# Performance work log

Measured on AMD Instinct MI355X. Metric: run time of the kernel, lower is better.

The kernel has to match this reference:

```python
import jax, jax.numpy as jnp
import numpy as np
from jax import lax

KSIZE, STRIDE, RATE, FUSE_K, SCALE, FUSE = 3, 1, 2, 3, 10.0, True


def _same_pad(h, w, k, s):
    oh, ow = -(-h // s), -(-w // s)
    ph = max(0, (oh - 1) * s + k - h)
    pw = max(0, (ow - 1) * s + k - w)
    return (ph // 2, ph - ph // 2), (pw // 2, pw - pw // 2), oh, ow


def extract_patches(x, k, s):
    # x: [B,C,H,W] -> ([B, L, C, k, k], Ho, Wo); matches torch Unfold with 'same' padding
    B, C, H, W = x.shape
    (pt, pb), (pl, pr), Ho, Wo = _same_pad(H, W, k, s)
    xp = jnp.pad(x, ((0, 0), (0, 0), (pt, pb), (pl, pr)))
    rows = []
    for i in range(k):
        cols = [xp[:, :, i:i + s * (Ho - 1) + 1:s, j:j + s * (Wo - 1) + 1:s] for j in range(k)]
        rows.append(jnp.stack(cols, axis=2))  # [B,C,k,Ho,Wo]
    pat = jnp.stack(rows, axis=2)  # [B,C,k,k,Ho,Wo]
    pat = pat.reshape(B, C, k, k, Ho * Wo).transpose(0, 4, 1, 2, 3)
    return pat, Ho, Wo


def setup_inputs() -> dict:
    key = jax.random.key(0)
    kf, kb = jax.random.split(key)
    f = jax.random.normal(kf, (2, 128, 64, 64), dtype=jnp.float32)
    b = jax.random.normal(kb, (2, 128, 64, 64), dtype=jnp.float32)
    mask = jnp.zeros((2, 1, 256, 256), dtype=jnp.float32)
    return {"f": f, "b": b, "mask": mask}


def _forward(f, b, mask):
    B, C, Hr, Wr = f.shape
    kernel = 2 * RATE
    # raw background patches used as deconv kernels: [B, L, C, 4, 4]
    raw_w, _, _ = extract_patches(b, kernel, RATE * STRIDE)
    # nearest 1/rate downsample (torch nearest picks every rate-th pixel)
    fd = f[:, :, ::RATE, ::RATE]
    bd = b[:, :, ::RATE, ::RATE]
    Hf, Wf = fd.shape[2], fd.shape[3]
    Hb, Wb = bd.shape[2], bd.shape[3]
    L = Hb * Wb
    w, _, _ = extract_patches(bd, KSIZE, STRIDE)  # [B, L, C, 3, 3]
    # mask -> validity per background patch (original uses batch 0's mask only)
    md = mask[:, :, ::4 * RATE, ::4 * RATE]
    m, _, _ = extract_patches(md, KSIZE, STRIDE)  # [B, L, 1, 3, 3]
    mm = (jnp.mean(m[0], axis=(1, 2, 3)) == 0.0).astype(f.dtype)  # [L]
    # l2-normalize patch kernels (escape_NaN added per element before sum, as in torch)
    wn = w / jnp.sqrt(jnp.sum(w * w + 1e-4, axis=(2, 3, 4), keepdims=True))
    # correlation conv == batched GEMM over extracted foreground patches
    fp, _, _ = extract_patches(fd, KSIZE, 1)  # [B, P=Hf*Wf, C, 3, 3]
    scores = jnp.einsum('bpckl,bqckl->bqp', fp, wn)  # [B, L, Hf*Wf]
    scores = scores.reshape(B, Hb, Wb, Hf, Wf)

    if FUSE:
        def fuse_diag(y2):  # conv with 3x3 identity kernel, same pad == 3 diagonal shifts
            yp = jnp.pad(y2, ((1, 1), (1, 1)))
            return yp[:-2, :-2] + yp[1:-1, 1:-1] + yp[2:, 2:]

        def fuse_one(s):  # [Hb,Wb,Hf,Wf]
            y = fuse_diag(s.reshape(Hb * Wb, Hf * Wf)).reshape(Hb, Wb, Hf, Wf)
            y = y.transpose(1, 0, 3, 2)
            y = fuse_diag(y.reshape(Wb * Hb, Wf * Hf)).reshape(Wb, Hb, Wf, Hf)
            return y.transpose(1, 0, 3, 2)

        scores = jax.vmap(fuse_one)(scores)

    yi = scores.reshape(B, L, Hf, Wf) * mm[None, :, None, None]
    yi = jax.nn.softmax(yi * SCALE, axis=1) * mm[None, :, None, None]

    # transposed conv with per-batch raw patches as kernels (stride=rate, padding=1), /4
    def deconv_one(attn, wpat):  # attn [L,Hf,Wf], wpat [L,C,4,4]
        rhs = jnp.flip(wpat, axis=(2, 3)).transpose(1, 0, 2, 3)  # [C, L, 4, 4]
        pad = kernel - 1 - 1  # equivalent VALID padding for transposed conv with padding=1
        out = lax.conv_general_dilated(attn[None], rhs, (1, 1),
                                       padding=((pad, pad), (pad, pad)),
                                       lhs_dilation=(RATE, RATE),
                                       dimension_numbers=('NCHW', 'OIHW', 'NCHW'))
        return out[0] / 4.0

    y = jax.vmap(deconv_one)(yi, raw_w)  # [B, C, Hr, Wr]
    return y


def reference(f, b, mask):
    return _forward(f, b, mask)
```

## Files before the change

kernel.cpp:

```cpp
#include <hip/hip_runtime.h>
#include <hip/hip_bf16.h>
#include <math.h>

constexpr int HS = 32;
constexpr int Lq = 1024;
constexpr int CN = 128;

typedef short bf16x8 __attribute__((ext_vector_type(8)));
typedef float f32x4  __attribute__((ext_vector_type(4)));

__device__ inline unsigned short f2bf(float x) {
    union { float f; unsigned int u; } c; c.f = x;
    return (unsigned short)((c.u + 0x7FFF + ((c.u >> 16) & 1)) >> 16);
}
__device__ inline float bf2f(unsigned short h) {
    union { unsigned int u; float f; } c; c.u = ((unsigned int)h) << 16;
    return c.f;
}

__global__ __launch_bounds__(64) void k_prep2(const float* __restrict__ f,
                                              const float* __restrict__ bsrc,
                                              unsigned short* __restrict__ fH, unsigned short* __restrict__ fL,
                                              unsigned short* __restrict__ bH, unsigned short* __restrict__ bL,
                                              float* __restrict__ ssq) {
    int u = blockIdx.x;
    int tx = threadIdx.x;
    int p = u & (Lq - 1), bb = u >> 10;
    int py = p >> 5, px = p & 31;
    long srcbase = (((long)bb * CN) * 64 + 2 * py) * 64 + 2 * px;
    float s = 0.f;
#pragma unroll
    for (int i = 0; i < 2; ++i) {
        int c = tx + i * 64;
        long src = srcbase + (long)c * 4096;
        float fv = f[src], bv = bsrc[src];
        int o = u * CN + c;
        unsigned short fh = f2bf(fv), bh = f2bf(bv);
        fH[o] = fh; fL[o] = f2bf(fv - bf2f(fh));
        bH[o] = bh; bL[o] = f2bf(bv - bf2f(bh));
        s += bv * bv;
    }
    for (int off = 32; off > 0; off >>= 1) s += __shfl_down(s, off, 64);
    if (tx == 0) ssq[u] = s;
}

__global__ __launch_bounds__(256) void k_nm(const float* __restrict__ ssq, const float* __restrict__ mask,
                                            float* __restrict__ norms, float* __restrict__ mmb) {
    int idx = blockIdx.x * 256 + threadIdx.x;
    if (idx < 2048) {
        int q = idx & (Lq - 1);
        int bb = idx >> 10;
        int qy = q >> 5, qx = q & 31;
        float s = 0.1152f;
        for (int dk = -1; dk <= 1; ++dk) {
            int y = qy + dk; if ((unsigned)y >= (unsigned)HS) continue;
            for (int dl = -1; dl <= 1; ++dl) {
                int x = qx + dl; if ((unsigned)x >= (unsigned)HS) continue;
                s += ssq[bb * Lq + y * HS + x];
            }
        }
        norms[idx] = sqrtf(s);
    } else {
        int q = idx - 2048;
        int qy = q >> 5, qx = q & 31;
        float s = 0.f;
        for (int dk = -1; dk <= 1; ++dk) {
            int y = qy + dk; if ((unsigned)y >= (unsigned)HS) continue;
            for (int dl = -1; dl <= 1; ++dl) {
                int x = qx + dl; if ((unsigned)x >= (unsigned)HS) continue;
                s += mask[(8 * y) * 256 + 8 * x];
            }
        }
        mmb[q] = (s == 0.0f) ? 1.0f : 0.0f;
    }
}

__global__ __launch_bounds__(256) void k_gram(const unsigned short* __restrict__ fH,
                                              const unsigned short* __restrict__ fL,
                                              const unsigned short* __restrict__ bH,
                                              const unsigned short* __restrict__ bL,
                                              float* __restrict__ GT) {
    const long bz = blockIdx.z;
    const unsigned short* AH = fH + bz * 131072;
    const unsigned short* AL = fL + bz * 131072;
    const unsigned short* BH = bH + bz * 131072;
    const unsigned short* BL = bL + bz * 131072;
    float* C = GT + (bz << 20);
    int t = threadIdx.x, w = t >> 6, lane = t & 63, quad = lane >> 4, l16 = lane & 15;
    int wm = blockIdx.x * 64 + (w & 1) * 32;
    int wn = blockIdx.y * 64 + (w >> 1) * 32;
    int ko = quad * 8;
    f32x4 acc[2][2] = {};
#pragma unroll
    for (int k0 = 0; k0 < 128; k0 += 32) {
        bf16x8 ah0 = *(const bf16x8*)&AH[(wm + l16) * 128 + ko + k0];
        bf16x8 ah1 = *(const bf16x8*)&AH[(wm + 16 + l16) * 128 + ko + k0];
        bf16x8 al0 = *(const bf16x8*)&AL[(wm + l16) * 128 + ko + k0];
        bf16x8 al1 = *(const bf16x8*)&AL[(wm + 16 + l16) * 128 + ko + k0];
        bf16x8 bh0 = *(const bf16x8*)&BH[(wn + l16) * 128 + ko + k0];
        bf16x8 bh1 = *(const bf16x8*)&BH[(wn + 16 + l16) * 128 + ko + k0];
        bf16x8 bl0 = *(const bf16x8*)&BL[(wn + l16) * 128 + ko + k0];
        bf16x8 bl1 = *(const bf16x8*)&BL[(wn + 16 + l16) * 128 + ko + k0];
        acc[0][0] = __builtin_amdgcn_mfma_f32_16x16x32_bf16(ah0, bh0, acc[0][0], 0, 0, 0);
        acc[0][1] = __builtin_amdgcn_mfma_f32_16x16x32_bf16(ah0, bh1, acc[0][1], 0, 0, 0);
        acc[1][0] = __builtin_amdgcn_mfma_f32_16x16x32_bf16(ah1, bh0, acc[1][0], 0, 0, 0);
        acc[1][1] = __builtin_amdgcn_mfma_f32_16x16x32_bf16(ah1, bh1, acc[1][1], 0, 0, 0);
        acc[0][0] = __builtin_amdgcn_mfma_f32_16x16x32_bf16(ah0, bl0, acc[0][0], 0, 0, 0);
        acc[0][1] = __builtin_amdgcn_mfma_f32_16x16x32_bf16(ah0, bl1, acc[0][1], 0, 0, 0);
        acc[1][0] = __builtin_amdgcn_mfma_f32_16x16x32_bf16(ah1, bl0, acc[1][0], 0, 0, 0);
        acc[1][1] = __builtin_amdgcn_mfma_f32_16x16x32_bf16(ah1, bl1, acc[1][1], 0, 0, 0);
        acc[0][0] = __builtin_amdgcn_mfma_f32_16x16x32_bf16(al0, bh0, acc[0][0], 0, 0, 0);
        acc[0][1] = __builtin_amdgcn_mfma_f32_16x16x32_bf16(al0, bh1, acc[0][1], 0, 0, 0);
        acc[1][0] = __builtin_amdgcn_mfma_f32_16x16x32_bf16(al1, bh0, acc[1][0], 0, 0, 0);
        acc[1][1] = __builtin_amdgcn_mfma_f32_16x16x32_bf16(al1, bh1, acc[1][1], 0, 0, 0);
    }
#pragma unroll
    for (int i = 0; i < 2; ++i)
#pragma unroll
        for (int j = 0; j < 2; ++j) {
            int mrow = wm + i * 16 + quad * 4;
            int ncol = wn + j * 16 + l16;
#pragma unroll
            for (int r = 0; r < 4; ++r)
                C[(long)(mrow + r) * Lq + ncol] = acc[i][j][r];
        }
}

__global__ __launch_bounds__(256) void k_s0T(const float* __restrict__ GT, const float* __restrict__ norms,
                                             float* __restrict__ S0T) {
    int idx = blockIdx.x * 256 + threadIdx.x;
    int q  = idx & (Lq - 1);
    int pp = (idx >> 10) & (Lq - 1);
    int bb = idx >> 20;
    int qy = q >> 5, qx = q & 31, py = pp >> 5, px = pp & 31;
    const float* Gb = GT + ((long)bb << 20);
    float s = 0.f;
#pragma unroll
    for (int dk = -1; dk <= 1; ++dk) {
        if ((unsigned)(qy + dk) >= (unsigned)HS || (unsigned)(py + dk) >= (unsigned)HS) continue;
#pragma unroll
        for (int dl = -1; dl <= 1; ++dl) {
            if ((unsigned)(qx + dl) >= (unsigned)HS || (unsigned)(px + dl) >= (unsigned)HS) continue;
            int sft = dk * HS + dl;
            s += Gb[(long)(pp + sft) * Lq + (q + sft)];
        }
    }
    S0T[idx] = s / norms[bb * Lq + q];
}

__global__ __launch_bounds__(256) void k_fuse12(const float* __restrict__ S0, float* __restrict__ S2) {
    int idx = blockIdx.x * 256 + threadIdx.x;
    int p  = idx & (Lq - 1);
    int q  = (idx >> 10) & (Lq - 1);
    int bb = idx >> 20;
    int hb = q >> 5, wb = q & 31, hf = p >> 5, wf = p & 31;
    int ip = wb * HS + hb, jp = wf * HS + hf;
    const float* S = S0 + (long)bb * Lq * Lq;
    float s = 0.f;
#pragma unroll
    for (int d = -1; d <= 1; ++d) {
        int t = ip + d, r = jp + d;
        if ((unsigned)t < (unsigned)Lq && (unsigned)r < (unsigned)Lq) {
            int q2 = (t & 31) * HS + (t >> 5);
            int p2 = (r & 31) * HS + (r >> 5);
            long base = (long)q2 * Lq + p2;
            float v = S[base];
            if (q2 > 0 && p2 > 0)             v += S[base - (Lq + 1)];
            if (q2 < Lq - 1 && p2 < Lq - 1)   v += S[base + (Lq + 1)];
            s += v;
        }
    }
    S2[idx] = s;
}

__global__ __launch_bounds__(256) void k_softmaxT(const float* __restrict__ S2T, const float* __restrict__ mmb,
                                                  unsigned short* __restrict__ At) {
    int wid = blockIdx.x * 4 + (threadIdx.x >> 6);
    int lane = threadIdx.x & 63;
    int bb = wid >> 10, p = wid & (Lq - 1);
    const float* row = S2T + ((long)bb << 20) + (long)p * Lq;
    unsigned short* orow = At + ((long)bb << 20) + (long)p * Lq;
    float x[16]; float mx = -1e30f;
#pragma unroll
    for (int i = 0; i < 16; ++i) {
        int q = i * 64 + lane;
        x[i] = row[q] * mmb[q] * 10.0f;
        mx = fmaxf(mx, x[i]);
    }
    for (int off = 32; off > 0; off >>= 1) mx = fmaxf(mx, __shfl_xor(mx, off, 64));
    float e[16]; float s = 0.f;
#pragma unroll
    for (int i = 0; i < 16; ++i) { e[i] = __expf(x[i] - mx); s += e[i]; }
    for (int off = 32; off > 0; off >>= 1) s += __shfl_xor(s, off, 64);
    float inv = 1.0f / s;
#pragma unroll
    for (int i = 0; i < 16; ++i) {
        int q = i * 64 + lane;
        orow[q] = f2bf(e[i] * mmb[q] * inv);
    }
}

__global__ __launch_bounds__(256) void k_wm(const float* __restrict__ bsrc, unsigned short* __restrict__ Wm) {
    int idx = blockIdx.x * 256 + threadIdx.x;
    int q  = idx & (Lq - 1);
    int m  = (idx >> 10) & 2047;
    int bb = idx >> 21;
    int c = m >> 4, u = (m >> 2) & 3, v = m & 3;
    int qy = q >> 5, qx = q & 31;
    int y = 2 * qy + u - 1, x = 2 * qx + v - 1;
    float val = 0.f;
    if ((unsigned)y < 64u && (unsigned)x < 64u)
        val = bsrc[(((long)bb * CN + c) * 64 + y) * 64 + x];
    Wm[idx] = f2bf(val);
}

__global__ __launch_bounds__(256) void k_gemm_mfma(const unsigned short* __restrict__ WmA,
                                                   const unsigned short* __restrict__ At,
                                                   float* __restrict__ Cm) {
    const long bz = blockIdx.z;
    const unsigned short* A = WmA + bz * (2048L * Lq);
    const unsigned short* B = At  + bz * ((long)Lq * Lq);
    float* C = Cm + bz * (2048L * Lq);
    __shared__ __align__(16) unsigned short Bs[4096];
    int t = threadIdx.x;
    int w = t >> 6, lane = t & 63;
    int quad = lane >> 4, l16 = lane & 15;
    int m0 = blockIdx.x * 64, n0 = blockIdx.y * 64;
    const unsigned short* aS = A + (long)(m0 + w * 16 + l16) * Lq + quad * 8;
    const unsigned short* bS = B + (long)(n0 + w * 16 + l16) * Lq + quad * 8;
    int sidx = w * 512 + quad * 128 + l16 * 8;
    int fidx = quad * 128 + l16 * 8;
    f32x4 acc0 = {0,0,0,0}, acc1 = {0,0,0,0}, acc2 = {0,0,0,0}, acc3 = {0,0,0,0};
    for (int k0 = 0; k0 < Lq; k0 += 64) {
        bf16x8 bv0 = *(const bf16x8*)(bS + k0);
        bf16x8 bv1 = *(const bf16x8*)(bS + k0 + 32);
        bf16x8 af0 = *(const bf16x8*)(aS + k0);
        bf16x8 af1 = *(const bf16x8*)(aS + k0 + 32);
        __syncthreads();
        *(bf16x8*)&Bs[sidx]        = bv0;
        *(bf16x8*)&Bs[2048 + sidx] = bv1;
        __syncthreads();
#pragma unroll
        for (int kc = 0; kc < 2; ++kc) {
            int o = kc * 2048;
            bf16x8 af = kc ? af1 : af0;
            bf16x8 b0 = *(const bf16x8*)&Bs[o + fidx];
            bf16x8 b1 = *(const bf16x8*)&Bs[o + 512 + fidx];
            bf16x8 b2 = *(const bf16x8*)&Bs[o + 1024 + fidx];
            bf16x8 b3 = *(const bf16x8*)&Bs[o + 1536 + fidx];
            acc0 = __builtin_amdgcn_mfma_f32_16x16x32_bf16(af, b0, acc0, 0, 0, 0);
            acc1 = __builtin_amdgcn_mfma_f32_16x16x32_bf16(af, b1, acc1, 0, 0, 0);
            acc2 = __builtin_amdgcn_mfma_f32_16x16x32_bf16(af, b2, acc2, 0, 0, 0);
            acc3 = __builtin_amdgcn_mfma_f32_16x16x32_bf16(af, b3, acc3, 0, 0, 0);
        }
    }
    int mrow = m0 + w * 16 + quad * 4;
#pragma unroll
    for (int r = 0; r < 4; ++r) {
        C[(long)(mrow + r) * Lq + n0 +  0 + l16] = acc0[r];
        C[(long)(mrow + r) * Lq + n0 + 16 + l16] = acc1[r];
        C[(long)(mrow + r) * Lq + n0 + 32 + l16] = acc2[r];
        C[(long)(mrow + r) * Lq + n0 + 48 + l16] = acc3[r];
    }
}

__global__ __launch_bounds__(256) void k_epi2(const float* __restrict__ P, float* __restrict__ out) {
    int idx = blockIdx.x * 256 + threadIdx.x;
    int ox = idx & 63, oy = (idx >> 6) & 63, c = (idx >> 12) & 127, bb = idx >> 19;
    const float* Pb = P + (long)bb * 2048 * Lq;
    float s = 0.f;
#pragma unroll
    for (int u = 0; u < 4; ++u) {
        int t = oy + u - 2;
        if (t & 1) continue;
        int iy = t >> 1;
        if ((unsigned)iy >= (unsigned)HS) continue;
#pragma unroll
        for (int v = 0; v < 4; ++v) {
            int r = ox + v - 2;
            if (r & 1) continue;
            int ix = r >> 1;
            if ((unsigned)ix >= (unsigned)HS) continue;
            s += Pb[(long)((c << 4) + (3 - u) * 4 + (3 - v)) * Lq + (iy << 5) + ix];
        }
    }
    out[idx] = 0.25f * s;
}

extern "C" void kernel_launch(void* const* d_in, const int* in_sizes, int n_in,
                              void* d_out, int out_size, void* d_ws, size_t ws_size,
                              hipStream_t stream) {
    const float* f    = (const float*)d_in[0];
    const float* bsrc = (const float*)d_in[1];
    const float* mask = (const float*)d_in[2];
    float* out = (float*)d_out;
    float* ws = (float*)d_ws;

    float* ssq   = ws;
    float* norms = ssq   + 2048;
    float* mmb   = norms + 2048;
    unsigned short* fH = (unsigned short*)(mmb + 1024);
    unsigned short* fL = fH + 262144;
    unsigned short* bH = fL + 262144;
    unsigned short* bL = bH + 262144;
    float* GTa   = (float*)(bL + 262144);
    float* C1    = GTa + 2097152;
    float* C2    = C1  + 2097152;
    unsigned short* Wm = (unsigned short*)(C2 + 2097152);
    float* S0T  = C1;
    float* S2T  = C2;
    unsigned short* attnT = (unsigned short*)GTa;
    float* P    = C1;

    hipLaunchKernelGGL(k_prep2,     dim3(2048),       dim3(64),  0, stream, f, bsrc, fH, fL, bH, bL, ssq);
    hipLaunchKernelGGL(k_nm,        dim3(12),         dim3(256), 0, stream, ssq, mask, norms, mmb);
    hipLaunchKernelGGL(k_gram,      dim3(16, 16, 2),  dim3(256), 0, stream, fH, fL, bH, bL, GTa);
    hipLaunchKernelGGL(k_s0T,       dim3(8192),       dim3(256), 0, stream, GTa, norms, S0T);
    hipLaunchKernelGGL(k_fuse12,    dim3(8192),       dim3(256), 0, stream, S0T, S2T);
    hipLaunchKernelGGL(k_softmaxT,  dim3(512),        dim3(256), 0, stream, S2T, mmb, attnT);
    hipLaunchKernelGGL(k_wm,        dim3(16384),      dim3(256), 0, stream, bsrc, Wm);
    hipLaunchKernelGGL(k_gemm_mfma, dim3(32, 16, 2),  dim3(256), 0, stream, Wm, attnT, P);
    hipLaunchKernelGGL(k_epi2,      dim3(4096),       dim3(256), 0, stream, P, out);
}
```

Before: 160.3 us.

## Fuse diagonal fuse into softmax and merge Wm build into prep kernel

Folds the k_fuse12 diagonal-sum stencil into the softmax kernel, so the S2T intermediate (8 MB fp32) is no longer written and re-read. It also merges the k_wm patch-matrix construction into the prep kernel as extra blocks, so there are two fewer launches. The risk is in the fused softmax: each lane now does strided, transposed gathers from S0T that are poorly coalesced, and only 512 blocks run that heavier work, which may cost more than the saved traffic.

```diff
diff --git a/kernel.cpp b/kernel.cpp
--- a/kernel.cpp
+++ b/kernel.cpp
@@ -18,30 +18,46 @@
     return c.f;
 }
 
-__global__ __launch_bounds__(64) void k_prep2(const float* __restrict__ f,
-                                              const float* __restrict__ bsrc,
-                                              unsigned short* __restrict__ fH, unsigned short* __restrict__ fL,
-                                              unsigned short* __restrict__ bH, unsigned short* __restrict__ bL,
-                                              float* __restrict__ ssq) {
-    int u = blockIdx.x;
+__global__ __launch_bounds__(256) void k_prep3(const float* __restrict__ f,
+                                               const float* __restrict__ bsrc,
+                                               unsigned short* __restrict__ fH, unsigned short* __restrict__ fL,
+                                               unsigned short* __restrict__ bH, unsigned short* __restrict__ bL,
+                                               float* __restrict__ ssq,
+                                               unsigned short* __restrict__ Wm) {
     int tx = threadIdx.x;
-    int p = u & (Lq - 1), bb = u >> 10;
-    int py = p >> 5, px = p & 31;
-    long srcbase = (((long)bb * CN) * 64 + 2 * py) * 64 + 2 * px;
-    float s = 0.f;
-#pragma unroll
-    for (int i = 0; i < 2; ++i) {
-        int c = tx + i * 64;
-        long src = srcbase + (long)c * 4096;
-        float fv = f[src], bv = bsrc[src];
-        int o = u * CN + c;
-        unsigned short fh = f2bf(fv), bh = f2bf(bv);
-        fH[o] = fh; fL[o] = f2bf(fv - bf2f(fh));
-        bH[o] = bh; bL[o] = f2bf(bv - bf2f(bh));
-        s += bv * bv;
-    }
-    for (int off = 32; off > 0; off >>= 1) s += __shfl_down(s, off, 64);
-    if (tx == 0) ssq[u] = s;
+    if (blockIdx.x < 512) {
+        int u = blockIdx.x * 4 + (tx >> 6);
+        int lane = tx & 63;
+        int p = u & (Lq - 1), bb = u >> 10;
+        int py = p >> 5, px = p & 31;
+        long srcbase = (((long)bb * CN) * 64 + 2 * py) * 64 + 2 * px;
+        float s = 0.f;
+#pragma unroll
+        for (int i = 0; i < 2; ++i) {
+            int c = lane + i * 64;
+            long src = srcbase + (long)c * 4096;
+            float fv = f[src], bv = bsrc[src];
+            int o = u * CN + c;
+            unsigned short fh = f2bf(fv), bh = f2bf(bv);
+            fH[o] = fh; fL[o] = f2bf(fv - bf2f(fh));
+            bH[o] = bh; bL[o] = f2bf(bv - bf2f(bh));
+            s += bv * bv;
+        }
+        for (int off = 32; off > 0; off >>= 1) s += __shfl_down(s, off, 64);
+        if (lane == 0) ssq[u] = s;
+    } else {
+        int idx = (blockIdx.x - 512) * 256 + tx;
+        int q  = idx & (Lq - 1);
+        int m  = (idx >> 10) & 2047;
+        int bb = idx >> 21;
+        int c = m >> 4, u = (m >> 2) & 3, v = m & 3;
+        int qy = q >> 5, qx = q & 31;
+        int y = 2 * qy + u - 1, x = 2 * qx + v - 1;
+        float val = 0.f;
+        if ((unsigned)y < 64u && (unsigned)x < 64u)
+            val = bsrc[(((long)bb * CN + c) * 64 + y) * 64 + x];
+        Wm[idx] = f2bf(val);
+    }
 }
 
 __global__ __launch_bounds__(256) void k_nm(const float* __restrict__ ssq, const float* __restrict__ mask,
@@ -148,70 +164,49 @@
     S0T[idx] = s / norms[bb * Lq + q];
 }
 
-__global__ __launch_bounds__(256) void k_fuse12(const float* __restrict__ S0, float* __restrict__ S2) {
-    int idx = blockIdx.x * 256 + threadIdx.x;
-    int p  = idx & (Lq - 1);
-    int q  = (idx >> 10) & (Lq - 1);
-    int bb = idx >> 20;
-    int hb = q >> 5, wb = q & 31, hf = p >> 5, wf = p & 31;
-    int ip = wb * HS + hb, jp = wf * HS + hf;
-    const float* S = S0 + (long)bb * Lq * Lq;
-    float s = 0.f;
-#pragma unroll
-    for (int d = -1; d <= 1; ++d) {
-        int t = ip + d, r = jp + d;
-        if ((unsigned)t < (unsigned)Lq && (unsigned)r < (unsigned)Lq) {
-            int q2 = (t & 31) * HS + (t >> 5);
-            int p2 = (r & 31) * HS + (r >> 5);
-            long base = (long)q2 * Lq + p2;
-            float v = S[base];
-            if (q2 > 0 && p2 > 0)             v += S[base - (Lq + 1)];
-            if (q2 < Lq - 1 && p2 < Lq - 1)   v += S[base + (Lq + 1)];
-            s += v;
-        }
-    }
-    S2[idx] = s;
-}
-
-__global__ __launch_bounds__(256) void k_softmaxT(const float* __restrict__ S2T, const float* __restrict__ mmb,
-                                                  unsigned short* __restrict__ At) {
+__global__ __launch_bounds__(256) void k_fsm(const float* __restrict__ S0T, const float* __restrict__ mmb,
+                                             unsigned short* __restrict__ At) {
     int wid = blockIdx.x * 4 + (threadIdx.x >> 6);
     int lane = threadIdx.x & 63;
-    int bb = wid >> 10, p = wid & (Lq - 1);
-    const float* row = S2T + ((long)bb << 20) + (long)p * Lq;
-    unsigned short* orow = At + ((long)bb << 20) + (long)p * Lq;
+    int bb = wid >> 10, P = wid & (Lq - 1);
+    const float* S = S0T + ((long)bb << 20);
+    unsigned short* orow = At + ((long)bb << 20) + (long)P * Lq;
+    int hb = P >> 5, wb = P & 31;
+    int ip = wb * HS + hb;
     float x[16]; float mx = -1e30f;
 #pragma unroll
     for (int i = 0; i < 16; ++i) {
-        int q = i * 64 + lane;
-        x[i] = row[q] * mmb[q] * 10.0f;
+        int Q = i * 64 + lane;
+        int hf = Q >> 5, wf = Q & 31;
+        int jp = wf * HS + hf;
+        float s = 0.f;
+#pragma unroll
+        for (int d = -1; d <= 1; ++d) {
+            int t = ip + d, r = jp + d;
+            if ((unsigned)t < (unsigned)Lq && (unsigned)r < (unsigned)Lq) {
+                int q2 = (t & 31) * HS + (t >> 5);
+                int p2 = (r & 31) * HS + (r >> 5);
+                long base = (long)q2 * Lq + p2;
+                float v = S[base];
+                if (q2 > 0 && p2 > 0)             v += S[base - (Lq + 1)];
+                if (q2 < Lq - 1 && p2 < Lq - 1)   v += S[base + (Lq + 1)];
+                s += v;
+            }
+        }
+        x[i] = s * mmb[Q] * 10.0f;
         mx = fmaxf(mx, x[i]);
     }
     for (int off = 32; off > 0; off >>= 1) mx = fmaxf(mx, __shfl_xor(mx, off, 64));
-    float e[16]; float s = 0.f;
-#pragma unroll
-    for (int i = 0; i < 16; ++i) { e[i] = __expf(x[i] - mx); s += e[i]; }
-    for (int off = 32; off > 0; off >>= 1) s += __shfl_xor(s, off, 64);
-    float inv = 1.0f / s;
+    float e[16]; float sum = 0.f;
+#pragma unroll
+    for (int i = 0; i < 16; ++i) { e[i] = __expf(x[i] - mx); sum += e[i]; }
+    for (int off = 32; off > 0; off >>= 1) sum += __shfl_xor(sum, off, 64);
+    float inv = 1.0f / sum;
 #pragma unroll
     for (int i = 0; i < 16; ++i) {
-        int q = i * 64 + lane;
-        orow[q] = f2bf(e[i] * mmb[q] * inv);
-    }
-}
-
-__global__ __launch_bounds__(256) void k_wm(const float* __restrict__ bsrc, unsigned short* __restrict__ Wm) {
-    int idx = blockIdx.x * 256 + threadIdx.x;
-    int q  = idx & (Lq - 1);
-    int m  = (idx >> 10) & 2047;
-    int bb = idx >> 21;
-    int c = m >> 4, u = (m >> 2) & 3, v = m & 3;
-    int qy = q >> 5, qx = q & 31;
-    int y = 2 * qy + u - 1, x = 2 * qx + v - 1;
-    float val = 0.f;
-    if ((unsigned)y < 64u && (unsigned)x < 64u)
-        val = bsrc[(((long)bb * CN + c) * 64 + y) * 64 + x];
-    Wm[idx] = f2bf(val);
+        int Q = i * 64 + lane;
+        orow[Q] = f2bf(e[i] * mmb[Q] * inv);
+    }
 }
 
 __global__ __launch_bounds__(256) void k_gemm_mfma(const unsigned short* __restrict__ WmA,
@@ -308,17 +303,14 @@
     float* C2    = C1  + 2097152;
     unsigned short* Wm = (unsigned short*)(C2 + 2097152);
     float* S0T  = C1;
-    float* S2T  = C2;
     unsigned short* attnT = (unsigned short*)GTa;
     float* P    = C1;
 
-    hipLaunchKernelGGL(k_prep2,     dim3(2048),       dim3(64),  0, stream, f, bsrc, fH, fL, bH, bL, ssq);
+    hipLaunchKernelGGL(k_prep3,     dim3(16896),      dim3(256), 0, stream, f, bsrc, fH, fL, bH, bL, ssq, Wm);
     hipLaunchKernelGGL(k_nm,        dim3(12),         dim3(256), 0, stream, ssq, mask, norms, mmb);
     hipLaunchKernelGGL(k_gram,      dim3(16, 16, 2),  dim3(256), 0, stream, fH, fL, bH, bL, GTa);
     hipLaunchKernelGGL(k_s0T,       dim3(8192),       dim3(256), 0, stream, GTa, norms, S0T);
-    hipLaunchKernelGGL(k_fuse12,    dim3(8192),       dim3(256), 0, stream, S0T, S2T);
-    hipLaunchKernelGGL(k_softmaxT,  dim3(512),        dim3(256), 0, stream, S2T, mmb, attnT);
-    hipLaunchKernelGGL(k_wm,        dim3(16384),      dim3(256), 0, stream, bsrc, Wm);
+    hipLaunchKernelGGL(k_fsm,       dim3(512),        dim3(256), 0, stream, S0T, mmb, attnT);
     hipLaunchKernelGGL(k_gemm_mfma, dim3(32, 16, 2),  dim3(256), 0, stream, Wm, attnT, P);
     hipLaunchKernelGGL(k_epi2,      dim3(4096),       dim3(256), 0, stream, P, out);
 }
```

Measured after the change: 170.7 us. +6.5%, slower.
